# Kernel tuning notes

Measured on AMD Instinct MI355X. Metric: run time of the kernel, lower is better.

## Reference

```python
import jax, jax.numpy as jnp
import numpy as np
import math

N_EMBED = 2048
N_HEAD = 16
HEAD_DIM = N_EMBED // N_HEAD  # 128
ROPE_BASE = 10000.0


def _rope_tables(T, dim, dtype):
    # inv_freq over even indices, emb = concat(freqs, freqs) along last dim
    inv_freq = 1.0 / (ROPE_BASE ** (jnp.arange(0, dim, 2, dtype=jnp.float32) / dim))
    t = jnp.arange(T, dtype=jnp.float32)
    freqs = jnp.einsum('i,j->ij', t, inv_freq)          # [T, dim/2]
    emb = jnp.concatenate([freqs, freqs], axis=-1)      # [T, dim]
    return jnp.cos(emb).astype(dtype), jnp.sin(emb).astype(dtype)


def _rotate_half(x):
    h = x.shape[-1] // 2
    return jnp.concatenate([-x[..., h:], x[..., :h]], axis=-1)


def setup_inputs() -> dict:
    key = jax.random.key(0)
    ks = jax.random.split(key, 5)
    B, T, C = 32, 256, N_EMBED
    s = 1.0 / math.sqrt(C)
    return {
        'x': jax.random.normal(ks[0], (B, T, C), dtype=jnp.float32),
        'wq': jax.random.normal(ks[1], (C, C), dtype=jnp.float32) * s,
        'wk': jax.random.normal(ks[2], (C, C), dtype=jnp.float32) * s,
        'wv': jax.random.normal(ks[3], (C, C), dtype=jnp.float32) * s,
        'wo': jax.random.normal(ks[4], (C, C), dtype=jnp.float32) * s,
    }


def reference(x, wq, wk, wv, wo):
    B, T, C = x.shape
    H, D = N_HEAD, HEAD_DIM
    # torch Linear: y = x @ W^T
    q = (x @ wq.T).reshape(B, T, H, D).transpose(0, 2, 1, 3)  # [B,H,T,D]
    k = (x @ wk.T).reshape(B, T, H, D).transpose(0, 2, 1, 3)
    v = (x @ wv.T).reshape(B, T, H, D).transpose(0, 2, 1, 3)

    cos, sin = _rope_tables(T, D, x.dtype)  # [T,D] each, broadcast over B,H
    q = q * cos + _rotate_half(q) * sin
    k = k * cos + _rotate_half(k) * sin

    att = jnp.einsum('bhqd,bhkd->bhqk', q, k) / math.sqrt(D)
    causal = jnp.triu(jnp.ones((T, T), dtype=bool), k=1)
    att = jnp.where(causal, jnp.finfo(att.dtype).min, att)
    att = jax.nn.softmax(att, axis=-1)
    # dropout p=0.0 -> identity
    y = jnp.einsum('bhqk,bhkd->bhqd', att, v)
    y = y.transpose(0, 2, 1, 3).reshape(B, T, C)
    return y @ wo.T
```

## Files before the change

kernel.cpp:

```cpp
#include <hip/hip_runtime.h>

#define HB 32
#define HT 256
#define HC 2048
#define HH 16
#define HD 128
#define HM (HB * HT)

typedef __bf16 bf16x8 __attribute__((ext_vector_type(8)));
typedef float f32x4 __attribute__((ext_vector_type(4)));
typedef float f32x16 __attribute__((ext_vector_type(16)));

__device__ __forceinline__ unsigned short f2bf(float f) {
  unsigned u = __float_as_uint(f);
  u += 0x7FFFu + ((u >> 16) & 1u);
  return (unsigned short)(u >> 16);
}
__device__ __forceinline__ float bf2f(unsigned short h) {
  return __uint_as_float(((unsigned)h) << 16);
}

__global__ __launch_bounds__(256) void cvt_all(
    const float* __restrict__ x, const float* __restrict__ wq, const float* __restrict__ wk,
    const float* __restrict__ wv, const float* __restrict__ wo,
    unsigned short* __restrict__ xb, unsigned short* __restrict__ wqb,
    unsigned short* __restrict__ wkb, unsigned short* __restrict__ wvb,
    unsigned short* __restrict__ wob) {
  size_t i = (size_t)blockIdx.x * 256 + threadIdx.x;
  const float* src;
  unsigned short* dst;
  size_t off;
  if (i < 4194304) {
    src = x; dst = xb; off = i;
  } else {
    size_t j = i - 4194304;
    int w = (int)(j >> 20);
    off = j & 1048575;
    src = (w == 0) ? wq : (w == 1) ? wk : (w == 2) ? wv : wo;
    dst = (w == 0) ? wqb : (w == 1) ? wkb : (w == 2) ? wvb : wob;
  }
  float4 v = ((const float4*)src)[off];
  ushort4 o;
  o.x = f2bf(v.x); o.y = f2bf(v.y); o.z = f2bf(v.z); o.w = f2bf(v.w);
  ((ushort4*)dst)[off] = o;
}

__device__ __forceinline__ void gl_lds16(const unsigned short* g, unsigned short* l) {
  __builtin_amdgcn_global_load_lds((const __attribute__((address_space(1))) void*)g,
                                   (__attribute__((address_space(3))) void*)l, 16, 0, 0);
}

__device__ __forceinline__ void gemm_core_wide(const unsigned short* __restrict__ Ab,
                                               const unsigned short* __restrict__ Wb,
                                               unsigned short* lsA, unsigned short* lsB,
                                               f32x16 acc[2][4], int tid) {
  const int lane = tid & 63, wave = tid >> 6;
  const int l31 = lane & 31, half = lane >> 5;
  const int wr = wave >> 1, wc = wave & 1;
  for (int kt = 0; kt < HC / 64; ++kt) {
    __syncthreads();
#pragma unroll
    for (int i = 0; i < 4; i++) {
      int c = i * 256 + tid;
      int row = c >> 3, cc = c & 7;
      int gc = cc ^ (row & 7);
      gl_lds16(Ab + (size_t)row * HC + kt * 64 + gc * 8, lsA + c * 8);
    }
#pragma unroll
    for (int i = 0; i < 8; i++) {
      int c = i * 256 + tid;
      int row = c >> 3, cc = c & 7;
      int gc = cc ^ (row & 7);
      gl_lds16(Wb + (size_t)row * HC + kt * 64 + gc * 8, lsB + c * 8);
    }
    __syncthreads();
#pragma unroll
    for (int ks = 0; ks < 4; ++ks) {
      const int g = ks * 2 + half;
      bf16x8 af[2], bfr[4];
#pragma unroll
      for (int mi = 0; mi < 2; mi++) {
        int r = wr * 64 + mi * 32 + l31;
        int cc = g ^ (r & 7);
        af[mi] = *(const bf16x8*)(lsA + r * 64 + cc * 8);
      }
#pragma unroll
      for (int nj = 0; nj < 4; nj++) {
        int r = wc * 128 + nj * 32 + l31;
        int cc = g ^ (r & 7);
        bfr[nj] = *(const bf16x8*)(lsB + r * 64 + cc * 8);
      }
#pragma unroll
      for (int mi = 0; mi < 2; mi++)
#pragma unroll
        for (int nj = 0; nj < 4; nj++)
          acc[mi][nj] = __builtin_amdgcn_mfma_f32_32x32x16_bf16(af[mi], bfr[nj], acc[mi][nj], 0, 0, 0);
    }
  }
}

__global__ __launch_bounds__(256, 2) void gemm_out(const unsigned short* __restrict__ A,
                                                   const unsigned short* __restrict__ W,
                                                   float* __restrict__ outp) {
  __shared__ __align__(16) unsigned short lsA[128 * 64];
  __shared__ __align__(16) unsigned short lsB[256 * 64];
  const int tid = threadIdx.x;
  const int lane = tid & 63, wave = tid >> 6;
  const int l31 = lane & 31, half = lane >> 5;
  const int wr = wave >> 1, wc = wave & 1;
  const int bm = blockIdx.x, bn = blockIdx.y;

  f32x16 acc[2][4];
#pragma unroll
  for (int i = 0; i < 2; i++)
#pragma unroll
    for (int j = 0; j < 4; j++)
#pragma unroll
      for (int r = 0; r < 16; r++) acc[i][j][r] = 0.f;

  gemm_core_wide(A + (size_t)bm * 128 * HC, W + (size_t)bn * 256 * HC, lsA, lsB, acc, tid);

#pragma unroll
  for (int mi = 0; mi < 2; mi++)
#pragma unroll
    for (int nj = 0; nj < 4; nj++)
#pragma unroll
      for (int g = 0; g < 4; g++)
#pragma unroll
        for (int rr = 0; rr < 4; rr++) {
          int m = bm * 128 + wr * 64 + mi * 32 + rr + 8 * g + 4 * half;
          int n = bn * 256 + wc * 128 + nj * 32 + l31;
          outp[(size_t)m * HC + n] = acc[mi][nj][g * 4 + rr];
        }
}

__global__ __launch_bounds__(256, 2) void gemm_qkv(const unsigned short* __restrict__ A,
                                                    const unsigned short* __restrict__ W0,
                                                    const unsigned short* __restrict__ W1,
                                                    const unsigned short* __restrict__ W2,
                                                    unsigned short* __restrict__ Qo,
                                                    unsigned short* __restrict__ Ko,
                                                    unsigned short* __restrict__ Vto) {
  __shared__ __align__(16) unsigned short lsA[128 * 64];
  __shared__ __align__(16) unsigned short lsB[256 * 64];
  const int tid = threadIdx.x;
  const int lane = tid & 63, wave = tid >> 6;
  const int l31 = lane & 31, half = lane >> 5;
  const int wr = wave >> 1, wc = wave & 1;
  const int bm = blockIdx.x;
  const int which = blockIdx.y >> 3;
  const int bn = blockIdx.y & 7;

  f32x16 acc[2][4];
#pragma unroll
  for (int i = 0; i < 2; i++)
#pragma unroll
    for (int j = 0; j < 4; j++)
#pragma unroll
      for (int r = 0; r < 16; r++) acc[i][j][r] = 0.f;

  if (which < 2) {
    const unsigned short* W = (which == 0) ? W0 : W1;
    unsigned short* outp = (which == 0) ? Qo : Ko;
    gemm_core_wide(A + (size_t)bm * 128 * HC, W + (size_t)bn * 256 * HC, lsA, lsB, acc, tid);
    const int h = bn * 2 + wc;
#pragma unroll
    for (int nj = 0; nj < 2; nj++) {
      const int dlo = nj * 32 + l31;
      const float invf = __expf((float)dlo * (-0.14391156831212787f));
#pragma unroll
      for (int mi = 0; mi < 2; mi++)
#pragma unroll
        for (int g = 0; g < 4; g++)
#pragma unroll
          for (int rr = 0; rr < 4; rr++) {
            int m = bm * 128 + wr * 64 + mi * 32 + rr + 8 * g + 4 * half;
            int t = m & 255, b = m >> 8;
            float ang = (float)t * invf;
            float sn, cs;
            __sincosf(ang, &sn, &cs);
            int reg = g * 4 + rr;
            float lo = acc[mi][nj][reg], hi = acc[mi][nj + 2][reg];
            size_t base = (((size_t)b * HH + h) * HT + t) * HD;
            outp[base + dlo] = f2bf(lo * cs - hi * sn);
            outp[base + 64 + dlo] = f2bf(hi * cs + lo * sn);
          }
    }
  } else {
    int v = bn * 64 + bm;
    int tok = v & 31, ch = v >> 5;
    gemm_core_wide(W2 + (size_t)ch * 128 * HC, A + (size_t)tok * 256 * HC, lsA, lsB, acc, tid);
    const int b = tok, h = ch;
#pragma unroll
    for (int mi = 0; mi < 2; mi++)
#pragma unroll
      for (int nj = 0; nj < 4; nj++)
#pragma unroll
        for (int g = 0; g < 4; g++)
#pragma unroll
          for (int rr = 0; rr < 4; rr++) {
            int d = wr * 64 + mi * 32 + rr + 8 * g + 4 * half;
            int t = wc * 128 + nj * 32 + l31;
            Vto[(((size_t)b * HH + h) * HD + d) * HT + t] = f2bf(acc[mi][nj][g * 4 + rr]);
          }
  }
}

__global__ __launch_bounds__(256) void attn_kernel(const unsigned short* __restrict__ Q,
                                                   const unsigned short* __restrict__ K,
                                                   const unsigned short* __restrict__ Vt,
                                                   unsigned short* __restrict__ Y) {
  const int g = blockIdx.x;
  const int wq = 3 - (g >> 9);
  const int bh = g & 511;
  const int wave = threadIdx.x >> 6;
  const int lane = threadIdx.x & 63;
  const int quad = lane >> 4, l16 = lane & 15;

  const unsigned short* Qh = Q + (size_t)bh * HT * HD;
  const unsigned short* Kh = K + (size_t)bh * HT * HD;
  const unsigned short* Vh = Vt + (size_t)bh * HD * HT;

  __shared__ __align__(16) unsigned short P[4][16 * 72];
  unsigned short* Pw = P[wave];

  const int qrow = wq * 64 + wave * 16;

  bf16x8 qf[4];
#pragma unroll
  for (int ks = 0; ks < 4; ks++)
    qf[ks] = *(const bf16x8*)(Qh + (size_t)(qrow + l16) * HD + ks * 32 + quad * 8);

  f32x4 o[8];
#pragma unroll
  for (int di = 0; di < 8; di++) o[di] = f32x4{0.f, 0.f, 0.f, 0.f};
  float mrow[4], lrow[4];
#pragma unroll
  for (int r = 0; r < 4; r++) { mrow[r] = -1e30f; lrow[r] = 0.f; }

  const float scale = 0.088388347648318447f;

  for (int ct = 0; ct <= wq; ++ct) {
    f32x4 s[4];
#pragma unroll
    for (int ni = 0; ni < 4; ni++) s[ni] = f32x4{0.f, 0.f, 0.f, 0.f};
    const int nimax = (ct == wq) ? wave : 3;
#pragma unroll
    for (int ks = 0; ks < 4; ks++) {
#pragma unroll
      for (int ni = 0; ni < 4; ni++) {
        if (ni <= nimax) {
          bf16x8 kf = *(const bf16x8*)(Kh + (size_t)(ct * 64 + ni * 16 + l16) * HD + ks * 32 + quad * 8);
          s[ni] = __builtin_amdgcn_mfma_f32_16x16x32_bf16(qf[ks], kf, s[ni], 0, 0, 0);
        }
      }
    }
    if (ct == wq) {
#pragma unroll
      for (int ni = 0; ni < 4; ni++)
#pragma unroll
        for (int r = 0; r < 4; r++) {
          int qr = wave * 16 + quad * 4 + r;
          int kc = ni * 16 + l16;
          s[ni][r] = (kc <= qr) ? s[ni][r] * scale : -1e30f;
        }
    } else {
#pragma unroll
      for (int ni = 0; ni < 4; ni++)
#pragma unroll
        for (int r = 0; r < 4; r++) s[ni][r] *= scale;
    }
#pragma unroll
    for (int r = 0; r < 4; r++) {
      float v = fmaxf(fmaxf(s[0][r], s[1][r]), fmaxf(s[2][r], s[3][r]));
      v = fmaxf(v, __shfl_xor(v, 1, 64));
      v = fmaxf(v, __shfl_xor(v, 2, 64));
      v = fmaxf(v, __shfl_xor(v, 4, 64));
      v = fmaxf(v, __shfl_xor(v, 8, 64));
      float mnew = fmaxf(mrow[r], v);
      float alpha = __expf(mrow[r] - mnew);
      mrow[r] = mnew;
      float rs = 0.f;
#pragma unroll
      for (int ni = 0; ni < 4; ni++) {
        float e = __expf(s[ni][r] - mnew);
        s[ni][r] = e;
        rs += e;
      }
      rs += __shfl_xor(rs, 1, 64);
      rs += __shfl_xor(rs, 2, 64);
      rs += __shfl_xor(rs, 4, 64);
      rs += __shfl_xor(rs, 8, 64);
      lrow[r] = lrow[r] * alpha + rs;
#pragma unroll
      for (int di = 0; di < 8; di++) o[di][r] *= alpha;
    }
#pragma unroll
    for (int ni = 0; ni < 4; ni++)
#pragma unroll
      for (int r = 0; r < 4; r++)
        Pw[(quad * 4 + r) * 72 + ni * 16 + l16] = f2bf(s[ni][r]);
#pragma unroll
    for (int ks = 0; ks < 2; ks++) {
      bf16x8 pf = *(const bf16x8*)(Pw + (size_t)l16 * 72 + ks * 32 + quad * 8);
#pragma unroll
      for (int di = 0; di < 8; di++) {
        bf16x8 vf = *(const bf16x8*)(Vh + (size_t)(di * 16 + l16) * HT + ct * 64 + ks * 32 + quad * 8);
        o[di] = __builtin_amdgcn_mfma_f32_16x16x32_bf16(pf, vf, o[di], 0, 0, 0);
      }
    }
  }

  const int b = bh >> 4, h = bh & 15;
#pragma unroll
  for (int r = 0; r < 4; r++) {
    float inv = 1.f / lrow[r];
    int t = qrow + quad * 4 + r;
    size_t rowb = ((size_t)b * HT + t) * HC + h * HD;
#pragma unroll
    for (int di = 0; di < 8; di++)
      Y[rowb + di * 16 + l16] = f2bf(o[di][r] * inv);
  }
}

extern "C" void kernel_launch(void* const* d_in, const int* in_sizes, int n_in,
                              void* d_out, int out_size, void* d_ws, size_t ws_size,
                              hipStream_t stream) {
  const float* x  = (const float*)d_in[0];
  const float* wq = (const float*)d_in[1];
  const float* wk = (const float*)d_in[2];
  const float* wv = (const float*)d_in[3];
  const float* wo = (const float*)d_in[4];
  float* out = (float*)d_out;

  char* ws = (char*)d_ws;
  const size_t MB = (size_t)1 << 20;
  unsigned short* wqb = (unsigned short*)(ws + 0 * MB);
  unsigned short* wkb = (unsigned short*)(ws + 8 * MB);
  unsigned short* wvb = (unsigned short*)(ws + 16 * MB);
  unsigned short* wob = (unsigned short*)(ws + 24 * MB);
  unsigned short* xb  = (unsigned short*)(ws + 32 * MB);
  unsigned short* Qb  = (unsigned short*)(ws + 64 * MB);
  unsigned short* Kb  = (unsigned short*)(ws + 96 * MB);
  unsigned short* Vtb = (unsigned short*)(ws + 128 * MB);
  unsigned short* Yb  = xb;

  cvt_all<<<32768, 256, 0, stream>>>(x, wq, wk, wv, wo, xb, wqb, wkb, wvb, wob);

  gemm_qkv<<<dim3(HM / 128, 24), 256, 0, stream>>>(xb, wqb, wkb, wvb, Qb, Kb, Vtb);

  attn_kernel<<<2048, 256, 0, stream>>>(Qb, Kb, Vtb, Yb);

  gemm_out<<<dim3(HM / 128, HC / 256), 256, 0, stream>>>(Yb, wob, out);
}
```

Before: 512.4 us.

## Rewrite GEMMs as 256x256 tiles with 4-stage async LDS pipeline

Replaces the 128x256 single-buffered GEMM core with a 512-thread, 256x256-tile core using 16x16x32 MFMAs and a 4-deep ring of K=32 LDS stages prefetched with global_load_lds, gated by explicit vmcnt waits and one barrier per step. The goal is to overlap global loads with MFMA work, cut the per-step double barrier, and raise reuse per loaded byte. LDS use rises to 128KB per block, so occupancy may fall to one block per CU, and the grid shrinks to 32x24 and 32x8 blocks, which may leave CUs less evenly loaded.

```diff
diff --git a/kernel.cpp b/kernel.cpp
--- a/kernel.cpp
+++ b/kernel.cpp
@@ -9,15 +9,11 @@
 
 typedef __bf16 bf16x8 __attribute__((ext_vector_type(8)));
 typedef float f32x4 __attribute__((ext_vector_type(4)));
-typedef float f32x16 __attribute__((ext_vector_type(16)));
 
 __device__ __forceinline__ unsigned short f2bf(float f) {
   unsigned u = __float_as_uint(f);
   u += 0x7FFFu + ((u >> 16) & 1u);
   return (unsigned short)(u >> 16);
-}
-__device__ __forceinline__ float bf2f(unsigned short h) {
-  return __uint_as_float(((unsigned)h) << 16);
 }
 
 __global__ __launch_bounds__(256) void cvt_all(
@@ -50,159 +46,181 @@
                                    (__attribute__((address_space(3))) void*)l, 16, 0, 0);
 }
 
-__device__ __forceinline__ void gemm_core_wide(const unsigned short* __restrict__ Ab,
-                                               const unsigned short* __restrict__ Wb,
-                                               unsigned short* lsA, unsigned short* lsB,
-                                               f32x16 acc[2][4], int tid) {
-  const int lane = tid & 63, wave = tid >> 6;
-  const int l31 = lane & 31, half = lane >> 5;
-  const int wr = wave >> 1, wc = wave & 1;
-  for (int kt = 0; kt < HC / 64; ++kt) {
-    __syncthreads();
-#pragma unroll
-    for (int i = 0; i < 4; i++) {
-      int c = i * 256 + tid;
-      int row = c >> 3, cc = c & 7;
-      int gc = cc ^ (row & 7);
-      gl_lds16(Ab + (size_t)row * HC + kt * 64 + gc * 8, lsA + c * 8);
-    }
-#pragma unroll
-    for (int i = 0; i < 8; i++) {
-      int c = i * 256 + tid;
-      int row = c >> 3, cc = c & 7;
-      int gc = cc ^ (row & 7);
-      gl_lds16(Wb + (size_t)row * HC + kt * 64 + gc * 8, lsB + c * 8);
-    }
-    __syncthreads();
-#pragma unroll
-    for (int ks = 0; ks < 4; ++ks) {
-      const int g = ks * 2 + half;
-      bf16x8 af[2], bfr[4];
-#pragma unroll
-      for (int mi = 0; mi < 2; mi++) {
-        int r = wr * 64 + mi * 32 + l31;
-        int cc = g ^ (r & 7);
-        af[mi] = *(const bf16x8*)(lsA + r * 64 + cc * 8);
-      }
-#pragma unroll
-      for (int nj = 0; nj < 4; nj++) {
-        int r = wc * 128 + nj * 32 + l31;
-        int cc = g ^ (r & 7);
-        bfr[nj] = *(const bf16x8*)(lsB + r * 64 + cc * 8);
-      }
-#pragma unroll
-      for (int mi = 0; mi < 2; mi++)
-#pragma unroll
-        for (int nj = 0; nj < 4; nj++)
-          acc[mi][nj] = __builtin_amdgcn_mfma_f32_32x32x16_bf16(af[mi], bfr[nj], acc[mi][nj], 0, 0, 0);
-    }
-  }
-}
-
-__global__ __launch_bounds__(256, 2) void gemm_out(const unsigned short* __restrict__ A,
+__device__ __forceinline__ int nfcol(int wn, int nf) {
+  return (wn >> 1) * 128 + (wn & 1) * 32 + (nf & 1) * 16 + (nf >> 1) * 64;
+}
+
+__device__ __forceinline__ void stage_tile(const unsigned short* __restrict__ A,
+                                           const unsigned short* __restrict__ W,
+                                           unsigned short* dA, unsigned short* dW,
+                                           int kt, int tid) {
+#pragma unroll
+  for (int i = 0; i < 2; i++) {
+    int c = i * 512 + tid;
+    int row = c >> 2, slot = c & 3;
+    int gc = slot ^ ((row >> 1) & 3);
+    gl_lds16(A + (size_t)row * HC + kt * 32 + gc * 8, dA + c * 8);
+  }
+#pragma unroll
+  for (int i = 0; i < 2; i++) {
+    int c = i * 512 + tid;
+    int row = c >> 2, slot = c & 3;
+    int gc = slot ^ ((row >> 1) & 3);
+    gl_lds16(W + (size_t)row * HC + kt * 32 + gc * 8, dW + c * 8);
+  }
+}
+
+#define NTILES 64
+
+__device__ __forceinline__ void gemm_core8(const unsigned short* __restrict__ A,
+                                           const unsigned short* __restrict__ W,
+                                           unsigned short* lsA, unsigned short* lsB,
+                                           f32x4 acc[8][4], int tid) {
+  const int lane = tid & 63;
+  const int l16 = lane & 15, quad = lane >> 4;
+  const int wave = tid >> 6;
+  const int wm = wave >> 2, wn = wave & 3;
+
+  stage_tile(A, W, lsA, lsB, 0, tid);
+  stage_tile(A, W, lsA + 8192, lsB + 8192, 1, tid);
+  stage_tile(A, W, lsA + 16384, lsB + 16384, 2, tid);
+  asm volatile("s_waitcnt vmcnt(8)");
+  __builtin_amdgcn_s_barrier();
+
+  for (int t = 0; t < NTILES; ++t) {
+    const int cur = t & 3;
+    const unsigned short* cA = lsA + cur * 8192;
+    const unsigned short* cB = lsB + cur * 8192;
+    if (t + 3 < NTILES) {
+      const int nb = (t + 3) & 3;
+      stage_tile(A, W, lsA + nb * 8192, lsB + nb * 8192, t + 3, tid);
+    }
+    bf16x8 af[8], bfr[4];
+#pragma unroll
+    for (int mf = 0; mf < 8; mf++) {
+      int row = wm * 128 + mf * 16 + l16;
+      int slot = quad ^ ((row >> 1) & 3);
+      af[mf] = *(const bf16x8*)(cA + row * 32 + slot * 8);
+    }
+#pragma unroll
+    for (int nf = 0; nf < 4; nf++) {
+      int row = nfcol(wn, nf) + l16;
+      int slot = quad ^ ((row >> 1) & 3);
+      bfr[nf] = *(const bf16x8*)(cB + row * 32 + slot * 8);
+    }
+    __builtin_amdgcn_s_setprio(1);
+#pragma unroll
+    for (int mf = 0; mf < 8; mf++)
+#pragma unroll
+      for (int nf = 0; nf < 4; nf++)
+        acc[mf][nf] = __builtin_amdgcn_mfma_f32_16x16x32_bf16(af[mf], bfr[nf], acc[mf][nf], 0, 0, 0);
+    __builtin_amdgcn_s_setprio(0);
+    if (t < NTILES - 3) {
+      asm volatile("s_waitcnt vmcnt(8)");
+    } else if (t == NTILES - 3) {
+      asm volatile("s_waitcnt vmcnt(4)");
+    } else if (t == NTILES - 2) {
+      asm volatile("s_waitcnt vmcnt(0)");
+    }
+    __builtin_amdgcn_s_barrier();
+  }
+}
+
+__global__ __launch_bounds__(512, 2) void gemm_out(const unsigned short* __restrict__ A,
                                                    const unsigned short* __restrict__ W,
                                                    float* __restrict__ outp) {
-  __shared__ __align__(16) unsigned short lsA[128 * 64];
-  __shared__ __align__(16) unsigned short lsB[256 * 64];
+  __shared__ __align__(16) unsigned short lsA[32768];
+  __shared__ __align__(16) unsigned short lsB[32768];
   const int tid = threadIdx.x;
   const int lane = tid & 63, wave = tid >> 6;
-  const int l31 = lane & 31, half = lane >> 5;
-  const int wr = wave >> 1, wc = wave & 1;
+  const int l16 = lane & 15, quad = lane >> 4;
+  const int wm = wave >> 2, wn = wave & 3;
   const int bm = blockIdx.x, bn = blockIdx.y;
 
-  f32x16 acc[2][4];
-#pragma unroll
-  for (int i = 0; i < 2; i++)
-#pragma unroll
-    for (int j = 0; j < 4; j++)
-#pragma unroll
-      for (int r = 0; r < 16; r++) acc[i][j][r] = 0.f;
-
-  gemm_core_wide(A + (size_t)bm * 128 * HC, W + (size_t)bn * 256 * HC, lsA, lsB, acc, tid);
-
-#pragma unroll
-  for (int mi = 0; mi < 2; mi++)
-#pragma unroll
-    for (int nj = 0; nj < 4; nj++)
-#pragma unroll
-      for (int g = 0; g < 4; g++)
-#pragma unroll
-        for (int rr = 0; rr < 4; rr++) {
-          int m = bm * 128 + wr * 64 + mi * 32 + rr + 8 * g + 4 * half;
-          int n = bn * 256 + wc * 128 + nj * 32 + l31;
-          outp[(size_t)m * HC + n] = acc[mi][nj][g * 4 + rr];
-        }
-}
-
-__global__ __launch_bounds__(256, 2) void gemm_qkv(const unsigned short* __restrict__ A,
-                                                    const unsigned short* __restrict__ W0,
-                                                    const unsigned short* __restrict__ W1,
-                                                    const unsigned short* __restrict__ W2,
-                                                    unsigned short* __restrict__ Qo,
-                                                    unsigned short* __restrict__ Ko,
-                                                    unsigned short* __restrict__ Vto) {
-  __shared__ __align__(16) unsigned short lsA[128 * 64];
-  __shared__ __align__(16) unsigned short lsB[256 * 64];
+  f32x4 acc[8][4];
+#pragma unroll
+  for (int i = 0; i < 8; i++)
+#pragma unroll
+    for (int j = 0; j < 4; j++) acc[i][j] = f32x4{0.f, 0.f, 0.f, 0.f};
+
+  gemm_core8(A + (size_t)bm * 256 * HC, W + (size_t)bn * 256 * HC, lsA, lsB, acc, tid);
+
+#pragma unroll
+  for (int mf = 0; mf < 8; mf++)
+#pragma unroll
+    for (int nf = 0; nf < 4; nf++) {
+      const int n = bn * 256 + nfcol(wn, nf) + l16;
+#pragma unroll
+      for (int r = 0; r < 4; r++) {
+        const int m = bm * 256 + wm * 128 + mf * 16 + quad * 4 + r;
+        outp[(size_t)m * HC + n] = acc[mf][nf][r];
+      }
+    }
+}
+
+__global__ __launch_bounds__(512, 2) void gemm_qkv(const unsigned short* __restrict__ A,
+                                                   const unsigned short* __restrict__ W0,
+                                                   const unsigned short* __restrict__ W1,
+                                                   const unsigned short* __restrict__ W2,
+                                                   unsigned short* __restrict__ Qo,
+                                                   unsigned short* __restrict__ Ko,
+                                                   unsigned short* __restrict__ Vto) {
+  __shared__ __align__(16) unsigned short lsA[32768];
+  __shared__ __align__(16) unsigned short lsB[32768];
   const int tid = threadIdx.x;
   const int lane = tid & 63, wave = tid >> 6;
-  const int l31 = lane & 31, half = lane >> 5;
-  const int wr = wave >> 1, wc = wave & 1;
+  const int l16 = lane & 15, quad = lane >> 4;
+  const int wm = wave >> 2, wn = wave & 3;
   const int bm = blockIdx.x;
   const int which = blockIdx.y >> 3;
   const int bn = blockIdx.y & 7;
 
-  f32x16 acc[2][4];
-#pragma unroll
-  for (int i = 0; i < 2; i++)
-#pragma unroll
-    for (int j = 0; j < 4; j++)
-#pragma unroll
-      for (int r = 0; r < 16; r++) acc[i][j][r] = 0.f;
+  f32x4 acc[8][4];
+#pragma unroll
+  for (int i = 0; i < 8; i++)
+#pragma unroll
+    for (int j = 0; j < 4; j++) acc[i][j] = f32x4{0.f, 0.f, 0.f, 0.f};
 
   if (which < 2) {
     const unsigned short* W = (which == 0) ? W0 : W1;
     unsigned short* outp = (which == 0) ? Qo : Ko;
-    gemm_core_wide(A + (size_t)bm * 128 * HC, W + (size_t)bn * 256 * HC, lsA, lsB, acc, tid);
-    const int h = bn * 2 + wc;
-#pragma unroll
-    for (int nj = 0; nj < 2; nj++) {
-      const int dlo = nj * 32 + l31;
-      const float invf = __expf((float)dlo * (-0.14391156831212787f));
-#pragma unroll
-      for (int mi = 0; mi < 2; mi++)
-#pragma unroll
-        for (int g = 0; g < 4; g++)
-#pragma unroll
-          for (int rr = 0; rr < 4; rr++) {
-            int m = bm * 128 + wr * 64 + mi * 32 + rr + 8 * g + 4 * half;
-            int t = m & 255, b = m >> 8;
-            float ang = (float)t * invf;
-            float sn, cs;
-            __sincosf(ang, &sn, &cs);
-            int reg = g * 4 + rr;
-            float lo = acc[mi][nj][reg], hi = acc[mi][nj + 2][reg];
-            size_t base = (((size_t)b * HH + h) * HT + t) * HD;
-            outp[base + dlo] = f2bf(lo * cs - hi * sn);
-            outp[base + 64 + dlo] = f2bf(hi * cs + lo * sn);
-          }
+    gemm_core8(A + (size_t)bm * 256 * HC, W + (size_t)bn * 256 * HC, lsA, lsB, acc, tid);
+    const int h = bn * 2 + (wn >> 1);
+#pragma unroll
+    for (int p = 0; p < 2; p++) {
+      const int d = (wn & 1) * 32 + p * 16 + l16;
+      const float invf = __expf((float)d * (-0.14391156831212787f));
+#pragma unroll
+      for (int mf = 0; mf < 8; mf++)
+#pragma unroll
+        for (int r = 0; r < 4; r++) {
+          const int m = bm * 256 + wm * 128 + mf * 16 + quad * 4 + r;
+          const int t = m & 255, b = m >> 8;
+          float ang = (float)t * invf;
+          float sn, cs;
+          __sincosf(ang, &sn, &cs);
+          float lo = acc[mf][p][r], hi = acc[mf][p + 2][r];
+          size_t base = (((size_t)b * HH + h) * HT + t) * HD;
+          outp[base + d] = f2bf(lo * cs - hi * sn);
+          outp[base + 64 + d] = f2bf(hi * cs + lo * sn);
+        }
     }
   } else {
-    int v = bn * 64 + bm;
-    int tok = v & 31, ch = v >> 5;
-    gemm_core_wide(W2 + (size_t)ch * 128 * HC, A + (size_t)tok * 256 * HC, lsA, lsB, acc, tid);
-    const int b = tok, h = ch;
-#pragma unroll
-    for (int mi = 0; mi < 2; mi++)
-#pragma unroll
-      for (int nj = 0; nj < 4; nj++)
-#pragma unroll
-        for (int g = 0; g < 4; g++)
-#pragma unroll
-          for (int rr = 0; rr < 4; rr++) {
-            int d = wr * 64 + mi * 32 + rr + 8 * g + 4 * half;
-            int t = wc * 128 + nj * 32 + l31;
-            Vto[(((size_t)b * HH + h) * HD + d) * HT + t] = f2bf(acc[mi][nj][g * 4 + rr]);
-          }
+    const int tok = bm;
+    const int ch = bn;
+    gemm_core8(W2 + (size_t)ch * 256 * HC, A + (size_t)tok * 256 * HC, lsA, lsB, acc, tid);
+#pragma unroll
+    for (int mf = 0; mf < 8; mf++)
+#pragma unroll
+      for (int nf = 0; nf < 4; nf++) {
+        const int tcol = nfcol(wn, nf) + l16;
+#pragma unroll
+        for (int r = 0; r < 4; r++) {
+          const int cabs = ch * 256 + wm * 128 + mf * 16 + quad * 4 + r;
+          const int hh = cabs >> 7, d = cabs & 127;
+          Vto[(((size_t)tok * HH + hh) * HD + d) * HT + tcol] = f2bf(acc[mf][nf][r]);
+        }
+      }
   }
 }
 
@@ -347,9 +365,9 @@
 
   cvt_all<<<32768, 256, 0, stream>>>(x, wq, wk, wv, wo, xb, wqb, wkb, wvb, wob);
 
-  gemm_qkv<<<dim3(HM / 128, 24), 256, 0, stream>>>(xb, wqb, wkb, wvb, Qb, Kb, Vtb);
+  gemm_qkv<<<dim3(HM / 256, 24), 512, 0, stream>>>(xb, wqb, wkb, wvb, Qb, Kb, Vtb);
 
   attn_kernel<<<2048, 256, 0, stream>>>(Qb, Kb, Vtb, Yb);
 
-  gemm_out<<<dim3(HM / 128, HC / 256), 256, 0, stream>>>(Yb, wob, out);
-}
+  gemm_out<<<dim3(HM / 256, HC / 256), 512, 0, stream>>>(Yb, wob, out);
+}
```

After: 573.4 us. 11.9% more time.
